# Optimization experiments

Hardware: AMD Instinct MI355X
Metric: run time of the kernel (lower is better)

## Reference

```python
import jax, jax.numpy as jnp
import numpy as np

B, N, DM, H = 1, 2048, 1024, 16
CURV = 1.0  # hyperbolic curvature


def setup_inputs() -> dict:
    key = jax.random.key(0)
    ks = jax.random.split(key, 5)
    s = 1.0 / np.sqrt(DM)  # nn.Linear default init scale
    x = jax.random.normal(ks[0], (B, N, DM), dtype=jnp.float32)
    Wq = jax.random.uniform(ks[1], (DM, DM), jnp.float32, -s, s)
    Wk = jax.random.uniform(ks[2], (DM, DM), jnp.float32, -s, s)
    Wv = jax.random.uniform(ks[3], (DM, DM), jnp.float32, -s, s)
    Wo = jax.random.uniform(ks[4], (DM, DM), jnp.float32, -s, s)
    return {"x": x, "Wq": Wq, "Wk": Wk, "Wv": Wv, "Wo": Wo}


def reference(x, Wq, Wk, Wv, Wo):
    b, n, d = x.shape
    hd = d // H

    def split_heads(t):  # [B,N,D] -> [B,H,N,hd]
        return t.reshape(b, n, H, hd).transpose(0, 2, 1, 3)

    q = split_heads(x @ Wq.T)
    k = split_heads(x @ Wk.T)
    v = split_heads(x @ Wv.T)

    q_norm_sq = jnp.sum(q * q, axis=-1, keepdims=True)      # [B,H,N,1]
    k_norm_sq = jnp.sum(k * k, axis=-1)[:, :, None, :]      # [B,H,1,N]
    qk = jnp.einsum('bhnd,bhmd->bhnm', q, k)                # [B,H,N,N]

    diff_sq = jnp.maximum(q_norm_sq + k_norm_sq - 2.0 * qk, 0.0)
    denom = jnp.maximum((1.0 - CURV * q_norm_sq) * (1.0 - CURV * k_norm_sq), 1e-6)
    cosh_arg = jnp.maximum(1.0 + 2.0 * CURV * diff_sq / denom, 1.0)
    # safe acosh: acosh(1)=0; mask avoids inf grad at the boundary
    distance = jnp.where(cosh_arg > 1.0,
                         jnp.arccosh(jnp.maximum(cosh_arg, 1.0 + 1e-12)),
                         0.0)

    attn = jax.nn.softmax(-distance, axis=-1)               # [B,H,N,N]
    out = jnp.einsum('bhnm,bhmd->bhnd', attn, v)            # [B,H,N,hd]
    out = out.transpose(0, 2, 1, 3).reshape(b, n, d)
    return out @ Wo.T
```

## Files before the change

### kernel.cpp

```cpp
#include <hip/hip_runtime.h>
#include <math.h>

#define NSEQ   2048
#define DMODEL 1024
#define NHEADS 16
#define HD     64

typedef short bf16x8 __attribute__((ext_vector_type(8)));
typedef float f32x4  __attribute__((ext_vector_type(4)));
typedef unsigned short ushort8_t __attribute__((ext_vector_type(8)));

__device__ __forceinline__ unsigned short f2bf(float x) {
    unsigned int u = __builtin_bit_cast(unsigned int, x);
    unsigned int r = (u + 0x7FFFu + ((u >> 16) & 1u)) >> 16;
    return (unsigned short)r;
}

__global__ __launch_bounds__(256) void convert_inputs(
    const float* __restrict__ x,  const float* __restrict__ Wq,
    const float* __restrict__ Wk, const float* __restrict__ Wv,
    const float* __restrict__ Wo,
    unsigned short* __restrict__ xb, unsigned short* __restrict__ Wb,
    unsigned short* __restrict__ Wob)
{
    const size_t i8 = ((size_t)blockIdx.x * 256 + threadIdx.x) * 8;
    const float* src;
    unsigned short* dst;
    if (i8 < (2ull << 20)) {
        src = x + i8;  dst = xb + i8;
    } else if (i8 < (5ull << 20)) {
        const size_t o = i8 - (2ull << 20);
        const size_t s = o >> 20;
        src = (s == 0 ? Wq : (s == 1 ? Wk : Wv)) + (o & ((1u << 20) - 1));
        dst = Wb + o;
    } else {
        const size_t o = i8 - (5ull << 20);
        src = Wo + o;  dst = Wob + o;
    }
    const float4 v0 = *reinterpret_cast<const float4*>(src);
    const float4 v1 = *reinterpret_cast<const float4*>(src + 4);
    ushort8_t r;
    r[0] = f2bf(v0.x); r[1] = f2bf(v0.y); r[2] = f2bf(v0.z); r[3] = f2bf(v0.w);
    r[4] = f2bf(v1.x); r[5] = f2bf(v1.y); r[6] = f2bf(v1.z); r[7] = f2bf(v1.w);
    *reinterpret_cast<ushort8_t*>(dst) = r;
}

template <int QKV>
__global__ __launch_bounds__(256) void gemm_bt_bf16(
    const unsigned short* __restrict__ A, const unsigned short* __restrict__ B,
    float* __restrict__ C0,
    unsigned short* __restrict__ QbO, float* __restrict__ qnO,
    float* __restrict__ cq2O,
    unsigned short* __restrict__ KbO, float* __restrict__ knO,
    float* __restrict__ ckO,
    unsigned short* __restrict__ VbO)
{
    __shared__ unsigned short Ahs[128 * 64];
    __shared__ unsigned short Bhs[64 * 64];

    const int bm   = blockIdx.x * 128;
    const int bn   = blockIdx.y * 64;
    const int t    = threadIdx.x;
    const int wid  = t >> 6;
    const int lane = t & 63;
    const int g    = lane >> 4;
    const int r    = lane & 15;
    const int wm   = wid * 32;

    const int sel = QKV ? (bn >> 10) : 0;
    const int bnl = QKV ? (bn & 1023) : bn;

    f32x4 acc[2][4];
#pragma unroll
    for (int i = 0; i < 2; ++i)
#pragma unroll
        for (int j = 0; j < 4; ++j) acc[i][j] = (f32x4){0.f, 0.f, 0.f, 0.f};

    const int srowA = t >> 1;
    const int shalA = t & 1;
    const int srowB = t >> 2;
    const int squadB = t & 3;

    for (int k0 = 0; k0 < DMODEL; k0 += 64) {
        __syncthreads();
        ushort8_t av[4], bv[2];
#pragma unroll
        for (int c = 0; c < 4; ++c)
            av[c] = *reinterpret_cast<const ushort8_t*>(
                &A[(size_t)(bm + srowA) * DMODEL + k0 + shalA * 32 + c * 8]);
#pragma unroll
        for (int c = 0; c < 2; ++c)
            bv[c] = *reinterpret_cast<const ushort8_t*>(
                &B[(size_t)(bn + srowB) * DMODEL + k0 + (squadB * 2 + c) * 8]);
#pragma unroll
        for (int c = 0; c < 4; ++c) {
            const int sw = ((shalA * 4 + c) ^ (srowA & 7)) * 8;
            *reinterpret_cast<ushort8_t*>(&Ahs[srowA * 64 + sw]) = av[c];
        }
#pragma unroll
        for (int c = 0; c < 2; ++c) {
            const int sw = ((squadB * 2 + c) ^ (srowB & 7)) * 8;
            *reinterpret_cast<ushort8_t*>(&Bhs[srowB * 64 + sw]) = bv[c];
        }
        __syncthreads();

#pragma unroll
        for (int dc = 0; dc < 2; ++dc) {
            bf16x8 af[2], bfr[4];
#pragma unroll
            for (int mt = 0; mt < 2; ++mt)
                af[mt] = *reinterpret_cast<const bf16x8*>(
                    &Ahs[(wm + mt * 16 + r) * 64 + ((dc * 4 + g) ^ (r & 7)) * 8]);
#pragma unroll
            for (int nt = 0; nt < 4; ++nt)
                bfr[nt] = *reinterpret_cast<const bf16x8*>(
                    &Bhs[(nt * 16 + r) * 64 + ((dc * 4 + g) ^ (r & 7)) * 8]);
#pragma unroll
            for (int mt = 0; mt < 2; ++mt)
#pragma unroll
                for (int nt = 0; nt < 4; ++nt)
                    acc[mt][nt] = __builtin_amdgcn_mfma_f32_16x16x32_bf16(
                        af[mt], bfr[nt], acc[mt][nt], 0, 0, 0);
        }
    }

    if (QKV) {
        if (sel < 2) {
            unsigned short* Hb = sel ? KbO : QbO;
            float* narr = sel ? knO : qnO;
            float* carr = sel ? ckO : cq2O;
            const int hh = bnl >> 6;
#pragma unroll
            for (int mt = 0; mt < 2; ++mt) {
#pragma unroll
                for (int rg = 0; rg < 4; ++rg) {
                    float ss = 0.f;
#pragma unroll
                    for (int nt = 0; nt < 4; ++nt) {
                        const float v = acc[mt][nt][rg];
                        ss = fmaf(v, v, ss);
                        Hb[(size_t)(bm + wm + mt * 16 + g * 4 + rg) * 1024 +
                           bnl + nt * 16 + r] = f2bf(v);
                    }
                    ss += __shfl_xor(ss, 1, 64);
                    ss += __shfl_xor(ss, 2, 64);
                    ss += __shfl_xor(ss, 4, 64);
                    ss += __shfl_xor(ss, 8, 64);
                    if (r == 0) {
                        const int row = bm + wm + mt * 16 + g * 4 + rg;
                        narr[hh * NSEQ + row] = ss;
                        carr[hh * NSEQ + row] = (sel ? 1.0f : 2.0f) / (1.0f - ss);
                    }
                }
            }
        } else {
#pragma unroll
            for (int mt = 0; mt < 2; ++mt)
#pragma unroll
                for (int nt = 0; nt < 4; ++nt)
#pragma unroll
                    for (int rg = 0; rg < 4; ++rg)
                        VbO[(size_t)(bm + wm + mt * 16 + g * 4 + rg) * 1024 +
                            bnl + nt * 16 + r] = f2bf(acc[mt][nt][rg]);
        }
    } else {
#pragma unroll
        for (int mt = 0; mt < 2; ++mt)
#pragma unroll
            for (int nt = 0; nt < 4; ++nt)
#pragma unroll
                for (int rg = 0; rg < 4; ++rg)
                    C0[(size_t)(bm + wm + mt * 16 + g * 4 + rg) * 1024 +
                       bnl + nt * 16 + r] = acc[mt][nt][rg];
    }
}

__global__ __launch_bounds__(256) void vt_kernel_bf16(
    const unsigned short* __restrict__ Vb, unsigned short* __restrict__ Vt)
{
    __shared__ unsigned short Vs[64 * 72];
    const int h   = blockIdx.y;
    const int n0  = blockIdx.x * 64;
    const int t   = threadIdx.x;
    const int row = t >> 2;
    const int seg = (t & 3) * 16;

    const unsigned short* src = Vb + (size_t)(n0 + row) * 1024 + h * HD + seg;
    *reinterpret_cast<ushort8_t*>(&Vs[row * 72 + seg]) =
        *reinterpret_cast<const ushort8_t*>(src);
    *reinterpret_cast<ushort8_t*>(&Vs[row * 72 + seg + 8]) =
        *reinterpret_cast<const ushort8_t*>(src + 8);
    __syncthreads();

    ushort8_t a, b;
#pragma unroll
    for (int c = 0; c < 8; ++c) a[c] = Vs[(seg + c) * 72 + row];
#pragma unroll
    for (int c = 0; c < 8; ++c) b[c] = Vs[(seg + 8 + c) * 72 + row];
    unsigned short* dst = Vt + (size_t)(h * HD + row) * NSEQ + n0 + seg;
    *reinterpret_cast<ushort8_t*>(dst)     = a;
    *reinterpret_cast<ushort8_t*>(dst + 8) = b;
}

__global__ __launch_bounds__(256) void hyp_attn_v3(
    const unsigned short* __restrict__ Qb, const unsigned short* __restrict__ Kb,
    const unsigned short* __restrict__ Vt,
    const float* __restrict__ qn_a, const float* __restrict__ cq2_a,
    const float* __restrict__ kn_a, const float* __restrict__ ck_a,
    float* __restrict__ Opart, float* __restrict__ lpart, int jspan)
{
    __shared__ unsigned short Khs[64 * 64];
    __shared__ unsigned short Vts[64 * 64];
    __shared__ unsigned short Ps[4][16 * 64];

    const int h    = blockIdx.y;
    const int n0   = blockIdx.x * 64;
    const int jh   = blockIdx.z;
    const int t    = threadIdx.x;
    const int wid  = t >> 6;
    const int lane = t & 63;
    const int g    = lane >> 4;
    const int r    = lane & 15;
    const int qb   = n0 + wid * 16;

    bf16x8 qf[2];
#pragma unroll
    for (int dc = 0; dc < 2; ++dc)
        qf[dc] = *reinterpret_cast<const bf16x8*>(
            Qb + (size_t)(qb + r) * DMODEL + h * HD + dc * 32 + g * 8);

    float qn_r[4], c2q[4];
#pragma unroll
    for (int rg = 0; rg < 4; ++rg) {
        qn_r[rg] = qn_a[h * NSEQ + qb + g * 4 + rg];
        c2q[rg]  = cq2_a[h * NSEQ + qb + g * 4 + rg];
    }

    f32x4 oacc[4];
#pragma unroll
    for (int nt = 0; nt < 4; ++nt) oacc[nt] = (f32x4){0.f, 0.f, 0.f, 0.f};
    float l_acc[4] = {0.f, 0.f, 0.f, 0.f};

    const int srow = t >> 2;
    const int c0   = (t & 3) * 2;
    const int sw0  = (c0 ^ (srow & 7)) * 8;
    const int sw1  = ((c0 + 1) ^ (srow & 7)) * 8;
    const int sg   = (t & 3) * 16;
    unsigned short* Pw = &Ps[wid][0];

    const int ntb = jspan >> 6;
    for (int tb = 0; tb < ntb; ++tb) {
        const int j0 = jh * jspan + tb * 64;
        __syncthreads();
        {
            const unsigned short* ks = Kb + (size_t)(j0 + srow) * DMODEL + h * HD + sg;
            const unsigned short* vs = Vt + (size_t)(h * HD + srow) * NSEQ + j0 + sg;
            *reinterpret_cast<ushort8_t*>(&Khs[srow * 64 + sw0]) =
                *reinterpret_cast<const ushort8_t*>(ks);
            *reinterpret_cast<ushort8_t*>(&Khs[srow * 64 + sw1]) =
                *reinterpret_cast<const ushort8_t*>(ks + 8);
            *reinterpret_cast<ushort8_t*>(&Vts[srow * 64 + sw0]) =
                *reinterpret_cast<const ushort8_t*>(vs);
            *reinterpret_cast<ushort8_t*>(&Vts[srow * 64 + sw1]) =
                *reinterpret_cast<const ushort8_t*>(vs + 8);
        }
        __syncthreads();

#pragma unroll
        for (int jt = 0; jt < 4; ++jt) {
            f32x4 sac = (f32x4){0.f, 0.f, 0.f, 0.f};
#pragma unroll
            for (int dc = 0; dc < 2; ++dc) {
                const bf16x8 kb = *reinterpret_cast<const bf16x8*>(
                    &Khs[(jt * 16 + r) * 64 + ((dc * 4 + g) ^ (r & 7)) * 8]);
                sac = __builtin_amdgcn_mfma_f32_16x16x32_bf16(qf[dc], kb, sac, 0, 0, 0);
            }
            const int jj = j0 + jt * 16 + r;
            const float kn_v = kn_a[h * NSEQ + jj];
            const float ck_v = ck_a[h * NSEQ + jj];
#pragma unroll
            for (int rg = 0; rg < 4; ++rg) {
                const float dsq = fmaf(-2.f, sac[rg], qn_r[rg] + kn_v);
                const float ca  = fmaxf(fmaf(dsq, c2q[rg] * ck_v, 1.f), 1.0f);
                const float s2  = fmaf(ca, ca, -1.f);
                const float wj  = ca - __builtin_amdgcn_sqrtf(s2);
                l_acc[rg] += wj;
                const int qrow = g * 4 + rg;
                Pw[qrow * 64 +
                   ((2 * jt + (r >> 3)) ^ (qrow & 7)) * 8 + (r & 7)] = f2bf(wj);
            }
        }

#pragma unroll
        for (int kc = 0; kc < 2; ++kc) {
            const bf16x8 pa = *reinterpret_cast<const bf16x8*>(
                &Pw[r * 64 + ((kc * 4 + g) ^ (r & 7)) * 8]);
#pragma unroll
            for (int nt = 0; nt < 4; ++nt) {
                const bf16x8 vb = *reinterpret_cast<const bf16x8*>(
                    &Vts[(nt * 16 + r) * 64 + ((kc * 4 + g) ^ (r & 7)) * 8]);
                oacc[nt] = __builtin_amdgcn_mfma_f32_16x16x32_bf16(pa, vb, oacc[nt], 0, 0, 0);
            }
        }
    }

#pragma unroll
    for (int rg = 0; rg < 4; ++rg) {
        l_acc[rg] += __shfl_xor(l_acc[rg], 1, 64);
        l_acc[rg] += __shfl_xor(l_acc[rg], 2, 64);
        l_acc[rg] += __shfl_xor(l_acc[rg], 4, 64);
        l_acc[rg] += __shfl_xor(l_acc[rg], 8, 64);
    }

    float* Op = Opart + (size_t)jh * NSEQ * DMODEL;
#pragma unroll
    for (int nt = 0; nt < 4; ++nt)
#pragma unroll
        for (int rg = 0; rg < 4; ++rg)
            Op[(size_t)(qb + g * 4 + rg) * DMODEL + h * HD + nt * 16 + r] =
                oacc[nt][rg];
    if (r == 0) {
#pragma unroll
        for (int rg = 0; rg < 4; ++rg)
            lpart[(jh * NHEADS + h) * NSEQ + qb + g * 4 + rg] = l_acc[rg];
    }
}

__global__ __launch_bounds__(256) void merge_kernel(
    const float* __restrict__ Opart, const float* __restrict__ lpart,
    unsigned short* __restrict__ Ob, int njh)
{
    const size_t i8 = ((size_t)blockIdx.x * 256 + threadIdx.x) * 8;
    if (i8 >= (size_t)NSEQ * DMODEL) return;
    const int n  = (int)(i8 >> 10);
    const int dm = (int)(i8 & 1023);
    const int h  = dm >> 6;
    float lsum = 0.f;
    for (int p = 0; p < njh; ++p)
        lsum += lpart[(p * NHEADS + h) * NSEQ + n];
    const float li = 1.0f / lsum;
    float s[8] = {0.f, 0.f, 0.f, 0.f, 0.f, 0.f, 0.f, 0.f};
    for (int p = 0; p < njh; ++p) {
        const float* Opp = Opart + (size_t)p * NSEQ * DMODEL + i8;
#pragma unroll
        for (int c = 0; c < 2; ++c) {
            const float4 a = *reinterpret_cast<const float4*>(Opp + c * 4);
            s[c * 4 + 0] += a.x; s[c * 4 + 1] += a.y;
            s[c * 4 + 2] += a.z; s[c * 4 + 3] += a.w;
        }
    }
    ushort8_t o;
#pragma unroll
    for (int c = 0; c < 8; ++c) o[c] = f2bf(s[c] * li);
    *reinterpret_cast<ushort8_t*>(Ob + i8) = o;
}

extern "C" void kernel_launch(void* const* d_in, const int* in_sizes, int n_in,
                              void* d_out, int out_size, void* d_ws, size_t ws_size,
                              hipStream_t stream)
{
    const float* x  = (const float*)d_in[0];
    const float* Wq = (const float*)d_in[1];
    const float* Wk = (const float*)d_in[2];
    const float* Wv = (const float*)d_in[3];
    const float* Wo = (const float*)d_in[4];
    float* out = (float*)d_out;

    char* ws = (char*)d_ws;
    const size_t MB = 1048576;
    unsigned short* xb   = (unsigned short*)(ws);
    unsigned short* Wb   = (unsigned short*)(ws + 4  * MB);
    unsigned short* Wob  = (unsigned short*)(ws + 10 * MB);
    unsigned short* Qbuf = (unsigned short*)(ws + 12 * MB);
    unsigned short* Kbuf = (unsigned short*)(ws + 16 * MB);
    unsigned short* Vb   = (unsigned short*)(ws + 20 * MB);
    unsigned short* Vt   = (unsigned short*)(ws + 24 * MB);
    float*          qn   = (float*)(ws + 28 * MB);
    float*          cq2  = qn  + NHEADS * NSEQ;
    float*          kn   = cq2 + NHEADS * NSEQ;
    float*          ck   = kn  + NHEADS * NSEQ;
    float*          Opart= (float*)(ws + 29 * MB);
    unsigned short* Ob   = xb;

    const int njh = (ws_size >= 63 * MB) ? 4 : 2;
    float* lpart = (float*)(ws + (29 + (size_t)njh * 8) * MB);
    const int jspan = NSEQ / njh;

    const dim3 blk(256);

    convert_inputs<<<3072, blk, 0, stream>>>(x, Wq, Wk, Wv, Wo, xb, Wb, Wob);

    gemm_bt_bf16<1><<<dim3(NSEQ / 128, 3072 / 64), blk, 0, stream>>>(
        xb, Wb, nullptr, Qbuf, qn, cq2, Kbuf, kn, ck, Vb);

    vt_kernel_bf16<<<dim3(NSEQ / 64, NHEADS), blk, 0, stream>>>(Vb, Vt);

    hyp_attn_v3<<<dim3(NSEQ / 64, NHEADS, njh), blk, 0, stream>>>(
        Qbuf, Kbuf, Vt, qn, cq2, kn, ck, Opart, lpart, jspan);

    merge_kernel<<<(NSEQ * DMODEL / 8 + 255) / 256, blk, 0, stream>>>(
        Opart, lpart, Ob, njh);

    gemm_bt_bf16<0><<<dim3(NSEQ / 128, DMODEL / 64), blk, 0, stream>>>(
        Ob, Wob, out, nullptr, nullptr, nullptr,
        nullptr, nullptr, nullptr, nullptr);
}
```

Baseline: 105.7 us.

## Register-prefetch next tiles in GEMM and attention, cache key norms in LDS

Global loads for the next K-slice (GEMM) and the next K/V tile (attention) are now issued into registers before the compute of the current tile, so memory latency overlaps with MFMA work. The attention kernel also stages per-key norm factors for its whole span in shared memory instead of reading them from global memory inside the inner loop. The split count is fixed at two and the merge kernel is specialised for it. This costs more registers and shared memory, which may lower occupancy, and it drops the four-way split that was used when the workspace was large.

```diff
diff --git a/kernel.cpp b/kernel.cpp
--- a/kernel.cpp
+++ b/kernel.cpp
@@ -5,6 +5,8 @@
 #define DMODEL 1024
 #define NHEADS 16
 #define HD     64
+#define NJH    2
+#define JSPAN  (NSEQ / NJH)
 
 typedef short bf16x8 __attribute__((ext_vector_type(8)));
 typedef float f32x4  __attribute__((ext_vector_type(4)));
@@ -81,17 +83,19 @@
     const int srowB = t >> 2;
     const int squadB = t & 3;
 
+    const unsigned short* Ag = &A[(size_t)(bm + srowA) * DMODEL + shalA * 32];
+    const unsigned short* Bg = &B[(size_t)(bn + srowB) * DMODEL + squadB * 16];
+
+    ushort8_t av[4], bv[2];
+#pragma unroll
+    for (int c = 0; c < 4; ++c)
+        av[c] = *reinterpret_cast<const ushort8_t*>(Ag + c * 8);
+#pragma unroll
+    for (int c = 0; c < 2; ++c)
+        bv[c] = *reinterpret_cast<const ushort8_t*>(Bg + c * 8);
+
     for (int k0 = 0; k0 < DMODEL; k0 += 64) {
         __syncthreads();
-        ushort8_t av[4], bv[2];
-#pragma unroll
-        for (int c = 0; c < 4; ++c)
-            av[c] = *reinterpret_cast<const ushort8_t*>(
-                &A[(size_t)(bm + srowA) * DMODEL + k0 + shalA * 32 + c * 8]);
-#pragma unroll
-        for (int c = 0; c < 2; ++c)
-            bv[c] = *reinterpret_cast<const ushort8_t*>(
-                &B[(size_t)(bn + srowB) * DMODEL + k0 + (squadB * 2 + c) * 8]);
 #pragma unroll
         for (int c = 0; c < 4; ++c) {
             const int sw = ((shalA * 4 + c) ^ (srowA & 7)) * 8;
@@ -101,6 +105,16 @@
         for (int c = 0; c < 2; ++c) {
             const int sw = ((squadB * 2 + c) ^ (srowB & 7)) * 8;
             *reinterpret_cast<ushort8_t*>(&Bhs[srowB * 64 + sw]) = bv[c];
+        }
+        if (k0 + 64 < DMODEL) {
+#pragma unroll
+            for (int c = 0; c < 4; ++c)
+                av[c] = *reinterpret_cast<const ushort8_t*>(
+                    Ag + k0 + 64 + c * 8);
+#pragma unroll
+            for (int c = 0; c < 2; ++c)
+                bv[c] = *reinterpret_cast<const ushort8_t*>(
+                    Bg + k0 + 64 + c * 8);
         }
         __syncthreads();
 
@@ -202,16 +216,18 @@
     *reinterpret_cast<ushort8_t*>(dst + 8) = b;
 }
 
-__global__ __launch_bounds__(256) void hyp_attn_v3(
+__global__ __launch_bounds__(256) void hyp_attn_v5(
     const unsigned short* __restrict__ Qb, const unsigned short* __restrict__ Kb,
     const unsigned short* __restrict__ Vt,
     const float* __restrict__ qn_a, const float* __restrict__ cq2_a,
     const float* __restrict__ kn_a, const float* __restrict__ ck_a,
-    float* __restrict__ Opart, float* __restrict__ lpart, int jspan)
+    float* __restrict__ Opart, float* __restrict__ lpart)
 {
     __shared__ unsigned short Khs[64 * 64];
     __shared__ unsigned short Vts[64 * 64];
     __shared__ unsigned short Ps[4][16 * 64];
+    __shared__ float kns[JSPAN];
+    __shared__ float cks[JSPAN];
 
     const int h    = blockIdx.y;
     const int n0   = blockIdx.x * 64;
@@ -235,6 +251,11 @@
         qn_r[rg] = qn_a[h * NSEQ + qb + g * 4 + rg];
         c2q[rg]  = cq2_a[h * NSEQ + qb + g * 4 + rg];
     }
+#pragma unroll
+    for (int i = 0; i < JSPAN / 256; ++i) {
+        kns[i * 256 + t] = kn_a[h * NSEQ + jh * JSPAN + i * 256 + t];
+        cks[i * 256 + t] = ck_a[h * NSEQ + jh * JSPAN + i * 256 + t];
+    }
 
     f32x4 oacc[4];
 #pragma unroll
@@ -248,21 +269,28 @@
     const int sg   = (t & 3) * 16;
     unsigned short* Pw = &Ps[wid][0];
 
-    const int ntb = jspan >> 6;
+    const unsigned short* Kg = Kb + (size_t)(jh * JSPAN + srow) * DMODEL + h * HD + sg;
+    const unsigned short* Vg = Vt + (size_t)(h * HD + srow) * NSEQ + jh * JSPAN + sg;
+
+    ushort8_t kr0 = *reinterpret_cast<const ushort8_t*>(Kg);
+    ushort8_t kr1 = *reinterpret_cast<const ushort8_t*>(Kg + 8);
+    ushort8_t vr0 = *reinterpret_cast<const ushort8_t*>(Vg);
+    ushort8_t vr1 = *reinterpret_cast<const ushort8_t*>(Vg + 8);
+
+    const int ntb = JSPAN / 64;
     for (int tb = 0; tb < ntb; ++tb) {
-        const int j0 = jh * jspan + tb * 64;
         __syncthreads();
-        {
-            const unsigned short* ks = Kb + (size_t)(j0 + srow) * DMODEL + h * HD + sg;
-            const unsigned short* vs = Vt + (size_t)(h * HD + srow) * NSEQ + j0 + sg;
-            *reinterpret_cast<ushort8_t*>(&Khs[srow * 64 + sw0]) =
-                *reinterpret_cast<const ushort8_t*>(ks);
-            *reinterpret_cast<ushort8_t*>(&Khs[srow * 64 + sw1]) =
-                *reinterpret_cast<const ushort8_t*>(ks + 8);
-            *reinterpret_cast<ushort8_t*>(&Vts[srow * 64 + sw0]) =
-                *reinterpret_cast<const ushort8_t*>(vs);
-            *reinterpret_cast<ushort8_t*>(&Vts[srow * 64 + sw1]) =
-                *reinterpret_cast<const ushort8_t*>(vs + 8);
+        *reinterpret_cast<ushort8_t*>(&Khs[srow * 64 + sw0]) = kr0;
+        *reinterpret_cast<ushort8_t*>(&Khs[srow * 64 + sw1]) = kr1;
+        *reinterpret_cast<ushort8_t*>(&Vts[srow * 64 + sw0]) = vr0;
+        *reinterpret_cast<ushort8_t*>(&Vts[srow * 64 + sw1]) = vr1;
+        if (tb + 1 < ntb) {
+            const unsigned short* kn_ = Kg + (size_t)(tb + 1) * 64 * DMODEL;
+            const unsigned short* vn_ = Vg + (tb + 1) * 64;
+            kr0 = *reinterpret_cast<const ushort8_t*>(kn_);
+            kr1 = *reinterpret_cast<const ushort8_t*>(kn_ + 8);
+            vr0 = *reinterpret_cast<const ushort8_t*>(vn_);
+            vr1 = *reinterpret_cast<const ushort8_t*>(vn_ + 8);
         }
         __syncthreads();
 
@@ -275,9 +303,9 @@
                     &Khs[(jt * 16 + r) * 64 + ((dc * 4 + g) ^ (r & 7)) * 8]);
                 sac = __builtin_amdgcn_mfma_f32_16x16x32_bf16(qf[dc], kb, sac, 0, 0, 0);
             }
-            const int jj = j0 + jt * 16 + r;
-            const float kn_v = kn_a[h * NSEQ + jj];
-            const float ck_v = ck_a[h * NSEQ + jj];
+            const int jl = tb * 64 + jt * 16 + r;
+            const float kn_v = kns[jl];
+            const float ck_v = cks[jl];
 #pragma unroll
             for (int rg = 0; rg < 4; ++rg) {
                 const float dsq = fmaf(-2.f, sac[rg], qn_r[rg] + kn_v);
@@ -328,30 +356,27 @@
 
 __global__ __launch_bounds__(256) void merge_kernel(
     const float* __restrict__ Opart, const float* __restrict__ lpart,
-    unsigned short* __restrict__ Ob, int njh)
+    unsigned short* __restrict__ Ob)
 {
     const size_t i8 = ((size_t)blockIdx.x * 256 + threadIdx.x) * 8;
     if (i8 >= (size_t)NSEQ * DMODEL) return;
     const int n  = (int)(i8 >> 10);
     const int dm = (int)(i8 & 1023);
     const int h  = dm >> 6;
-    float lsum = 0.f;
-    for (int p = 0; p < njh; ++p)
-        lsum += lpart[(p * NHEADS + h) * NSEQ + n];
-    const float li = 1.0f / lsum;
-    float s[8] = {0.f, 0.f, 0.f, 0.f, 0.f, 0.f, 0.f, 0.f};
-    for (int p = 0; p < njh; ++p) {
-        const float* Opp = Opart + (size_t)p * NSEQ * DMODEL + i8;
-#pragma unroll
-        for (int c = 0; c < 2; ++c) {
-            const float4 a = *reinterpret_cast<const float4*>(Opp + c * 4);
-            s[c * 4 + 0] += a.x; s[c * 4 + 1] += a.y;
-            s[c * 4 + 2] += a.z; s[c * 4 + 3] += a.w;
-        }
-    }
+    const float li = 1.0f / (lpart[h * NSEQ + n] +
+                             lpart[(NHEADS + h) * NSEQ + n]);
+    const float* O0 = Opart + i8;
+    const float* O1 = Opart + (size_t)NSEQ * DMODEL + i8;
     ushort8_t o;
 #pragma unroll
-    for (int c = 0; c < 8; ++c) o[c] = f2bf(s[c] * li);
+    for (int c = 0; c < 2; ++c) {
+        const float4 a = *reinterpret_cast<const float4*>(O0 + c * 4);
+        const float4 b = *reinterpret_cast<const float4*>(O1 + c * 4);
+        o[c * 4 + 0] = f2bf((a.x + b.x) * li);
+        o[c * 4 + 1] = f2bf((a.y + b.y) * li);
+        o[c * 4 + 2] = f2bf((a.z + b.z) * li);
+        o[c * 4 + 3] = f2bf((a.w + b.w) * li);
+    }
     *reinterpret_cast<ushort8_t*>(Ob + i8) = o;
 }
 
@@ -380,11 +405,8 @@
     float*          kn   = cq2 + NHEADS * NSEQ;
     float*          ck   = kn  + NHEADS * NSEQ;
     float*          Opart= (float*)(ws + 29 * MB);
+    float*          lpart= (float*)(ws + 45 * MB);
     unsigned short* Ob   = xb;
-
-    const int njh = (ws_size >= 63 * MB) ? 4 : 2;
-    float* lpart = (float*)(ws + (29 + (size_t)njh * 8) * MB);
-    const int jspan = NSEQ / njh;
 
     const dim3 blk(256);
 
@@ -395,11 +417,11 @@
 
     vt_kernel_bf16<<<dim3(NSEQ / 64, NHEADS), blk, 0, stream>>>(Vb, Vt);
 
-    hyp_attn_v3<<<dim3(NSEQ / 64, NHEADS, njh), blk, 0, stream>>>(
-        Qbuf, Kbuf, Vt, qn, cq2, kn, ck, Opart, lpart, jspan);
+    hyp_attn_v5<<<dim3(NSEQ / 64, NHEADS, NJH), blk, 0, stream>>>(
+        Qbuf, Kbuf, Vt, qn, cq2, kn, ck, Opart, lpart);
 
     merge_kernel<<<(NSEQ * DMODEL / 8 + 255) / 256, blk, 0, stream>>>(
-        Opart, lpart, Ob, njh);
+        Opart, lpart, Ob);
 
     gemm_bt_bf16<0><<<dim3(NSEQ / 128, DMODEL / 64), blk, 0, stream>>>(
         Ob, Wob, out, nullptr, nullptr, nullptr,
```

Measured after the change: 95.08 us. 10.1% less time.
